# Kernel tuning notes

Measured on AMD Instinct MI355X. Metric: run time of the kernel, lower is better.

## Reference

```python
import jax, jax.numpy as jnp
import numpy as np

N_NODES = 100000


def gcn_conv(x, edge_index, W, b, n_nodes):
    """PyG GCNConv: add self-loops, symmetric deg^-1/2 normalization,
    linear transform, scatter-add aggregate, bias."""
    src, dst = edge_index[0], edge_index[1]
    # add self-loops
    loop = jnp.arange(n_nodes, dtype=edge_index.dtype)
    src = jnp.concatenate([src, loop])
    dst = jnp.concatenate([dst, loop])
    # transform first (in_dim >= out_dim ordering used by PyG)
    h = x @ W  # [N, out]
    # symmetric normalization from in-degree (incl. self-loops)
    ones = jnp.ones(src.shape[0], dtype=x.dtype)
    deg = jax.ops.segment_sum(ones, dst, num_segments=n_nodes)
    dinv = jnp.where(deg > 0, jax.lax.rsqrt(deg), 0.0).astype(x.dtype)
    norm = dinv[src] * dinv[dst]  # [E+N]
    msg = h[src] * norm[:, None]  # gather + scale
    out = jax.ops.segment_sum(msg, dst, num_segments=n_nodes)
    return out + b


def setup_inputs() -> dict:
    key = jax.random.key(0)
    k1, k2, k3, k4 = jax.random.split(key, 4)
    n, e = N_NODES, 1600000
    d_in, d_hid, n_cls = 256, 256, 64
    x = jax.random.normal(k1, (n, d_in), dtype=jnp.float32)
    edge_index = jax.random.randint(k2, (2, e), 0, n, dtype=jnp.int64)
    W1 = jax.random.normal(k3, (d_in, d_hid), dtype=jnp.float32) / np.sqrt(d_in)
    b1 = jnp.zeros((d_hid,), dtype=jnp.float32)
    W2 = jax.random.normal(k4, (d_hid, n_cls), dtype=jnp.float32) / np.sqrt(d_hid)
    b2 = jnp.zeros((n_cls,), dtype=jnp.float32)
    return {"x": x, "edge_index": edge_index, "W1": W1, "b1": b1, "W2": W2, "b2": b2}


def reference(x, edge_index, W1, b1, W2, b2):
    n = x.shape[0]
    h = jax.nn.relu(gcn_conv(x, edge_index, W1, b1, n))
    # dropout is identity in eval mode (training=False)
    logits = gcn_conv(h, edge_index, W2, b2, n)
    return jax.nn.log_softmax(logits, axis=1)
```

## Files before the change

kernel.cpp:

```cpp
#include <hip/hip_runtime.h>
#include <math.h>


typedef __attribute__((ext_vector_type(8))) short bf16x8;
typedef __attribute__((ext_vector_type(4))) float f32x4;

__device__ inline unsigned short f2bf(float f) {
    union { float f; unsigned int u; } v; v.f = f;
    unsigned int r = v.u + 0x7fffu + ((v.u >> 16) & 1u);
    return (unsigned short)(r >> 16);
}
__device__ inline float bf2f_lo(unsigned int u) {
    union { unsigned int u; float f; } v; v.u = u << 16; return v.f;
}
__device__ inline float bf2f_hi(unsigned int u) {
    union { unsigned int u; float f; } v; v.u = u & 0xffff0000u; return v.f;
}

__device__ inline void acc8(float* acc, uint4 q, float w) {
    acc[0] += bf2f_lo(q.x) * w; acc[1] += bf2f_hi(q.x) * w;
    acc[2] += bf2f_lo(q.y) * w; acc[3] += bf2f_hi(q.y) * w;
    acc[4] += bf2f_lo(q.z) * w; acc[5] += bf2f_hi(q.z) * w;
    acc[6] += bf2f_lo(q.w) * w; acc[7] += bf2f_hi(q.w) * w;
}

__global__ __launch_bounds__(256) void deg_rank_kernel(
    const int* __restrict__ dst, int E, int* __restrict__ cnt,
    int* __restrict__ rank) {
    int e = blockIdx.x * blockDim.x + threadIdx.x;
    if (e < E) rank[e] = atomicAdd(&cnt[dst[e]], 1);
}

__global__ __launch_bounds__(256) void scan_part1_kernel(
    const int* __restrict__ cnt, int* __restrict__ bsum, int N) {
    __shared__ int s[256];
    const int tid = threadIdx.x;
    int base = blockIdx.x * 1024 + tid * 4;
    int v = 0;
#pragma unroll
    for (int j = 0; j < 4; ++j)
        if (base + j < N) v += cnt[base + j];
    s[tid] = v;
    __syncthreads();
    for (int off = 128; off > 0; off >>= 1) {
        if (tid < off) s[tid] += s[tid + off];
        __syncthreads();
    }
    if (tid == 0) bsum[blockIdx.x] = s[0];
}

__global__ __launch_bounds__(1024) void scan_part2_kernel(
    const int* __restrict__ bsum, int* __restrict__ boffs, int NB,
    int* __restrict__ row_ptr, int N) {
    __shared__ int s[1024];
    const int tid = threadIdx.x;
    int v = (tid < NB) ? bsum[tid] : 0;
    s[tid] = v;
    __syncthreads();
    for (int off = 1; off < 1024; off <<= 1) {
        int t = (tid >= off) ? s[tid - off] : 0;
        __syncthreads();
        if (tid >= off) s[tid] += t;
        __syncthreads();
    }
    if (tid < NB) boffs[tid] = s[tid] - v;
    if (tid == 1023) row_ptr[N] = s[1023];
}

__global__ __launch_bounds__(256) void scan_part3_kernel(
    const int* __restrict__ cnt, const int* __restrict__ boffs,
    int* __restrict__ row_ptr, int N) {
    __shared__ int s[256];
    const int tid = threadIdx.x;
    int base = blockIdx.x * 1024 + tid * 4;
    int c[4];
    int v = 0;
#pragma unroll
    for (int j = 0; j < 4; ++j) {
        c[j] = (base + j < N) ? cnt[base + j] : 0;
        v += c[j];
    }
    s[tid] = v;
    __syncthreads();
    for (int off = 1; off < 256; off <<= 1) {
        int t = (tid >= off) ? s[tid - off] : 0;
        __syncthreads();
        if (tid >= off) s[tid] += t;
        __syncthreads();
    }
    int run = boffs[blockIdx.x] + s[tid] - v;
#pragma unroll
    for (int j = 0; j < 4; ++j) {
        if (base + j < N) {
            row_ptr[base + j] = run;
            run += c[j];
        }
    }
}

__global__ __launch_bounds__(256) void scatter_kernel(
    const int* __restrict__ src, const int* __restrict__ dst,
    const int* __restrict__ rank, const int* __restrict__ cnt,
    const int* __restrict__ row_ptr, int2* __restrict__ csr_ew, int E) {
    int e = blockIdx.x * blockDim.x + threadIdx.x;
    if (e >= E) return;
    int s = src[e], d = dst[e];
    float w = rsqrtf((float)cnt[s] + 1.0f) * rsqrtf((float)cnt[d] + 1.0f);
    int pos = row_ptr[d] + rank[e];
    int2 rec;
    rec.x = s;
    rec.y = __float_as_int(w);
    csr_ew[pos] = rec;
}

__global__ __launch_bounds__(256) void castw_kernel(
    const float* __restrict__ W1, const float* __restrict__ W2,
    unsigned short* __restrict__ W1t, unsigned short* __restrict__ W2t) {
    int i = blockIdx.x * 256 + threadIdx.x;
    if (i < 65536) {
        int n = i >> 8, k = i & 255;
        W1t[i] = f2bf(W1[(size_t)k * 256 + n]);
    } else if (i < 65536 + 16384) {
        int j = i - 65536;
        int n = j >> 8, k = j & 255;
        W2t[j] = f2bf(W2[(size_t)k * 64 + n]);
    }
}

__global__ __launch_bounds__(256) void gemm1_kernel(
    const float* __restrict__ A, const unsigned short* __restrict__ Bt,
    unsigned short* __restrict__ C, int M) {
    __shared__ unsigned short As[128][32];
    __shared__ unsigned short Bs[256][32];

    const int tid = threadIdx.x;
    const int wave = tid >> 6, lane = tid & 63;
    const int quad = lane >> 4, l15 = lane & 15;
    const int m0 = blockIdx.x * 128;

    f32x4 acc[8][4] = {};

    const int arow = tid >> 1;
    const int akk  = (tid & 1) << 4;
    const int gr = m0 + arow;

    for (int k0 = 0; k0 < 256; k0 += 32) {
        float4 a0 = make_float4(0.f,0.f,0.f,0.f), a1 = a0, a2 = a0, a3 = a0;
        if (gr < M) {
            const float* ap = &A[(size_t)gr * 256 + k0 + akk];
            a0 = *(const float4*)&ap[0];
            a1 = *(const float4*)&ap[4];
            a2 = *(const float4*)&ap[8];
            a3 = *(const float4*)&ap[12];
        }
        bf16x8 av0, av1;
        av0[0] = (short)f2bf(a0.x); av0[1] = (short)f2bf(a0.y);
        av0[2] = (short)f2bf(a0.z); av0[3] = (short)f2bf(a0.w);
        av0[4] = (short)f2bf(a1.x); av0[5] = (short)f2bf(a1.y);
        av0[6] = (short)f2bf(a1.z); av0[7] = (short)f2bf(a1.w);
        av1[0] = (short)f2bf(a2.x); av1[1] = (short)f2bf(a2.y);
        av1[2] = (short)f2bf(a2.z); av1[3] = (short)f2bf(a2.w);
        av1[4] = (short)f2bf(a3.x); av1[5] = (short)f2bf(a3.y);
        av1[6] = (short)f2bf(a3.z); av1[7] = (short)f2bf(a3.w);
        *(bf16x8*)&As[arow][akk]     = av0;
        *(bf16x8*)&As[arow][akk + 8] = av1;

        const unsigned short* bsrc = &Bt[(size_t)tid * 256 + k0];
        *(bf16x8*)&Bs[tid][0]  = *(const bf16x8*)&bsrc[0];
        *(bf16x8*)&Bs[tid][8]  = *(const bf16x8*)&bsrc[8];
        *(bf16x8*)&Bs[tid][16] = *(const bf16x8*)&bsrc[16];
        *(bf16x8*)&Bs[tid][24] = *(const bf16x8*)&bsrc[24];
        __syncthreads();

        bf16x8 bfv[4];
#pragma unroll
        for (int nt = 0; nt < 4; ++nt)
            bfv[nt] = *(const bf16x8*)&Bs[wave * 64 + nt * 16 + l15][quad * 8];
#pragma unroll
        for (int mt = 0; mt < 8; ++mt) {
            bf16x8 af = *(const bf16x8*)&As[mt * 16 + l15][quad * 8];
#pragma unroll
            for (int nt = 0; nt < 4; ++nt)
                acc[mt][nt] = __builtin_amdgcn_mfma_f32_16x16x32_bf16(
                    af, bfv[nt], acc[mt][nt], 0, 0, 0);
        }
        __syncthreads();
    }

#pragma unroll
    for (int mt = 0; mt < 8; ++mt) {
#pragma unroll
        for (int nt = 0; nt < 4; ++nt) {
            int gcol = wave * 64 + nt * 16 + l15;
#pragma unroll
            for (int r = 0; r < 4; ++r) {
                int grow = m0 + mt * 16 + quad * 4 + r;
                if (grow < M)
                    C[(size_t)grow * 256 + gcol] = f2bf(acc[mt][nt][r]);
            }
        }
    }
}

__global__ __launch_bounds__(256) void aggfused_kernel(
    const uint4* __restrict__ h,
    const int2* __restrict__ ew,
    const int* __restrict__ row_ptr, const int* __restrict__ cnt,
    const float* __restrict__ bias, const unsigned short* __restrict__ W2t,
    unsigned short* __restrict__ h2b, int N) {
    __shared__ unsigned short As[16][264];

    const int tid = threadIdx.x;
    const int wave = tid >> 6, lane = tid & 63;
    const int half = lane >> 5;
    const int c = lane & 31;
    const int node0 = blockIdx.x * 16;

    for (int i = 0; i < 4; ++i) {
        const int local = wave * 4 + i;
        const int node = node0 + local;
        float acc[8] = {0.f, 0.f, 0.f, 0.f, 0.f, 0.f, 0.f, 0.f};
        if (node < N) {
            float dv = rsqrtf((float)cnt[node] + 1.0f);
            float w0 = dv * dv;
            {
                uint4 q = h[(size_t)node * 32 + c];
                acc8(acc, q, half == 0 ? w0 : 0.f);
            }
            const int beg = row_ptr[node], end = row_ptr[node + 1];
            int e = beg;
            for (; e + 8 <= end; e += 8) {
                int2 r0 = ew[e + 0 + half];
                int2 r1 = ew[e + 2 + half];
                int2 r2 = ew[e + 4 + half];
                int2 r3 = ew[e + 6 + half];
                uint4 q0 = h[(size_t)r0.x * 32 + c];
                uint4 q1 = h[(size_t)r1.x * 32 + c];
                uint4 q2 = h[(size_t)r2.x * 32 + c];
                uint4 q3 = h[(size_t)r3.x * 32 + c];
                acc8(acc, q0, __int_as_float(r0.y));
                acc8(acc, q1, __int_as_float(r1.y));
                acc8(acc, q2, __int_as_float(r2.y));
                acc8(acc, q3, __int_as_float(r3.y));
            }
            for (; e < end; e += 2) {
                int idx = e + half;
                int idxc = min(idx, end - 1);
                int2 r = ew[idxc];
                float w = (idx < end) ? __int_as_float(r.y) : 0.f;
                uint4 q = h[(size_t)r.x * 32 + c];
                acc8(acc, q, w);
            }
        }
#pragma unroll
        for (int k = 0; k < 8; ++k) acc[k] += __shfl_xor(acc[k], 32, 64);

        if (half == 0) {
            float4 b0 = *(const float4*)&bias[c * 8];
            float4 b1 = *(const float4*)&bias[c * 8 + 4];
            unsigned int o0 = f2bf(fmaxf(acc[0] + b0.x, 0.f));
            unsigned int o1 = f2bf(fmaxf(acc[1] + b0.y, 0.f));
            unsigned int o2 = f2bf(fmaxf(acc[2] + b0.z, 0.f));
            unsigned int o3 = f2bf(fmaxf(acc[3] + b0.w, 0.f));
            unsigned int o4 = f2bf(fmaxf(acc[4] + b1.x, 0.f));
            unsigned int o5 = f2bf(fmaxf(acc[5] + b1.y, 0.f));
            unsigned int o6 = f2bf(fmaxf(acc[6] + b1.z, 0.f));
            unsigned int o7 = f2bf(fmaxf(acc[7] + b1.w, 0.f));
            uint4 ov;
            ov.x = o0 | (o1 << 16);
            ov.y = o2 | (o3 << 16);
            ov.z = o4 | (o5 << 16);
            ov.w = o6 | (o7 << 16);
            *(uint4*)&As[local][c * 8] = ov;
        }
    }
    __syncthreads();

    const int quad = lane >> 4, l15 = lane & 15;
    f32x4 accd = {};
#pragma unroll
    for (int k0 = 0; k0 < 8; ++k0) {
        bf16x8 af = *(const bf16x8*)&As[l15][k0 * 32 + quad * 8];
        bf16x8 bf = *(const bf16x8*)&W2t[(size_t)(wave * 16 + l15) * 256 +
                                         k0 * 32 + quad * 8];
        accd = __builtin_amdgcn_mfma_f32_16x16x32_bf16(af, bf, accd, 0, 0, 0);
    }
#pragma unroll
    for (int r = 0; r < 4; ++r) {
        int node = node0 + quad * 4 + r;
        if (node < N)
            h2b[(size_t)node * 64 + wave * 16 + l15] = f2bf(accd[r]);
    }
}

__global__ __launch_bounds__(256) void agg64_kernel(
    const uint4* __restrict__ h,
    const int2* __restrict__ ew, const int* __restrict__ row_ptr,
    const int* __restrict__ cnt, const float* __restrict__ bias,
    float* __restrict__ out, int N) {
    const int node = blockIdx.x * 4 + (threadIdx.x >> 6);
    if (node >= N) return;
    const int lane = threadIdx.x & 63;
    const int g = lane >> 3;
    const int c = lane & 7;

    float dv = rsqrtf((float)cnt[node] + 1.0f);
    float w0 = dv * dv;

    float acc[8] = {0.f, 0.f, 0.f, 0.f, 0.f, 0.f, 0.f, 0.f};
    {
        uint4 q = h[(size_t)node * 8 + c];
        acc8(acc, q, g == 0 ? w0 : 0.f);
    }

    const int beg = row_ptr[node], end = row_ptr[node + 1];
    int e = beg;
    for (; e + 16 <= end; e += 16) {
        int2 r0 = ew[e + g];
        int2 r1 = ew[e + 8 + g];
        uint4 q0 = h[(size_t)r0.x * 8 + c];
        uint4 q1 = h[(size_t)r1.x * 8 + c];
        acc8(acc, q0, __int_as_float(r0.y));
        acc8(acc, q1, __int_as_float(r1.y));
    }
    for (; e < end; e += 8) {
        int idx = e + g;
        int idxc = min(idx, end - 1);
        int2 r = ew[idxc];
        float w = (idx < end) ? __int_as_float(r.y) : 0.f;
        uint4 q = h[(size_t)r.x * 8 + c];
        acc8(acc, q, w);
    }

#pragma unroll
    for (int k = 0; k < 8; ++k) {
        acc[k] += __shfl_xor(acc[k], 8, 64);
        acc[k] += __shfl_xor(acc[k], 16, 64);
        acc[k] += __shfl_xor(acc[k], 32, 64);
    }

    float4 b0 = *(const float4*)&bias[c * 8];
    float4 b1 = *(const float4*)&bias[c * 8 + 4];
    float v[8];
    v[0] = acc[0] + b0.x; v[1] = acc[1] + b0.y;
    v[2] = acc[2] + b0.z; v[3] = acc[3] + b0.w;
    v[4] = acc[4] + b1.x; v[5] = acc[5] + b1.y;
    v[6] = acc[6] + b1.z; v[7] = acc[7] + b1.w;

    float m = v[0];
#pragma unroll
    for (int k = 1; k < 8; ++k) m = fmaxf(m, v[k]);
    m = fmaxf(m, __shfl_xor(m, 1, 64));
    m = fmaxf(m, __shfl_xor(m, 2, 64));
    m = fmaxf(m, __shfl_xor(m, 4, 64));
    float s = 0.f;
#pragma unroll
    for (int k = 0; k < 8; ++k) s += expf(v[k] - m);
    s += __shfl_xor(s, 1, 64);
    s += __shfl_xor(s, 2, 64);
    s += __shfl_xor(s, 4, 64);
    float ls = m + logf(s);

    if (g == 0) {
        float4 o0, o1;
        o0.x = v[0] - ls; o0.y = v[1] - ls; o0.z = v[2] - ls; o0.w = v[3] - ls;
        o1.x = v[4] - ls; o1.y = v[5] - ls; o1.z = v[6] - ls; o1.w = v[7] - ls;
        *(float4*)&out[(size_t)node * 64 + c * 8] = o0;
        *(float4*)&out[(size_t)node * 64 + c * 8 + 4] = o1;
    }
}

extern "C" void kernel_launch(void* const* d_in, const int* in_sizes, int n_in,
                              void* d_out, int out_size, void* d_ws, size_t ws_size,
                              hipStream_t stream) {
    const float* x  = (const float*)d_in[0];
    const int*   ei = (const int*)d_in[1];
    const float* W1 = (const float*)d_in[2];
    const float* b1 = (const float*)d_in[3];
    const float* W2 = (const float*)d_in[4];
    const float* b2 = (const float*)d_in[5];
    float* out = (float*)d_out;

    const int N = in_sizes[0] / 256;
    const int E = in_sizes[1] / 2;
    const int NP = 102400;
    const int NB = (N + 1023) / 1024;

    char* ws = (char*)d_ws;
    int*   cnt     = (int*)ws;                 ws += (size_t)NP * 4;
    int*   rank    = (int*)ws;                 ws += (size_t)E * 4;
    int*   row_ptr = (int*)ws;                 ws += (size_t)(NP + 4) * 4;
    int*   bsum    = (int*)ws;                 ws += (size_t)1024 * 4;
    int*   boffs   = (int*)ws;                 ws += (size_t)1024 * 4;
    int2*  csr_ew  = (int2*)ws;                ws += (size_t)E * 8;
    unsigned short* W1t   = (unsigned short*)ws; ws += (size_t)256 * 256 * 2;
    unsigned short* W2t   = (unsigned short*)ws; ws += (size_t)256 * 64 * 2;
    unsigned short* h1b   = (unsigned short*)ws; ws += (size_t)N * 256 * 2;
    unsigned short* h2b   = (unsigned short*)ws; ws += (size_t)N * 64 * 2;

    hipMemsetAsync(cnt, 0, (size_t)N * sizeof(int), stream);

    deg_rank_kernel<<<(E + 255) / 256, 256, 0, stream>>>(ei + E, E, cnt, rank);
    scan_part1_kernel<<<NB, 256, 0, stream>>>(cnt, bsum, N);
    scan_part2_kernel<<<1, 1024, 0, stream>>>(bsum, boffs, NB, row_ptr, N);
    scan_part3_kernel<<<NB, 256, 0, stream>>>(cnt, boffs, row_ptr, N);
    scatter_kernel<<<(E + 255) / 256, 256, 0, stream>>>(
        ei, ei + E, rank, cnt, row_ptr, csr_ew, E);

    castw_kernel<<<(65536 + 16384 + 255) / 256, 256, 0, stream>>>(W1, W2, W1t, W2t);

    gemm1_kernel<<<(N + 127) / 128, 256, 0, stream>>>(x, W1t, h1b, N);

    aggfused_kernel<<<(N + 15) / 16, 256, 0, stream>>>(
        (const uint4*)h1b, csr_ew, row_ptr, cnt, b1, W2t, h2b, N);

    agg64_kernel<<<(N + 3) / 4, 256, 0, stream>>>(
        (const uint4*)h2b, csr_ew, row_ptr, cnt, b2, out, N);
}
```

Measured before the change: 543.5 us.

## Aggregate bf16 x before W1 and fuse layer-1 GEMM into aggregation kernel

Reorders layer 1 to aggregate the bf16-cast input features first and then multiply by W1, which is valid because aggregation is linear. The separate GEMM kernel is removed: the x cast joins the weight-cast kernel, and the aggregation kernel now runs the W1 MFMA, bias+ReLU, and the W2 MFMA on each 16-node tile in shared memory. This drops the h1 write and read round-trip and one launch. In exchange each block re-reads W1t (128KB) from global/L2 per 16 nodes, and the bf16 rounding order changes.

```diff
diff --git a/kernel.cpp b/kernel.cpp
--- a/kernel.cpp
+++ b/kernel.cpp
@@ -113,102 +113,41 @@
     csr_ew[pos] = rec;
 }
 
-__global__ __launch_bounds__(256) void castw_kernel(
-    const float* __restrict__ W1, const float* __restrict__ W2,
-    unsigned short* __restrict__ W1t, unsigned short* __restrict__ W2t) {
+__global__ __launch_bounds__(256) void castxw_kernel(
+    const float* __restrict__ x, const float* __restrict__ W1,
+    const float* __restrict__ W2, unsigned int* __restrict__ xb,
+    unsigned short* __restrict__ W1t, unsigned short* __restrict__ W2t,
+    int NX8) {
     int i = blockIdx.x * 256 + threadIdx.x;
-    if (i < 65536) {
-        int n = i >> 8, k = i & 255;
-        W1t[i] = f2bf(W1[(size_t)k * 256 + n]);
-    } else if (i < 65536 + 16384) {
-        int j = i - 65536;
+    if (i < NX8) {
+        const float4* xp = (const float4*)&x[(size_t)i * 8];
+        float4 a0 = xp[0], a1 = xp[1];
+        uint4 o;
+        o.x = (unsigned int)f2bf(a0.x) | ((unsigned int)f2bf(a0.y) << 16);
+        o.y = (unsigned int)f2bf(a0.z) | ((unsigned int)f2bf(a0.w) << 16);
+        o.z = (unsigned int)f2bf(a1.x) | ((unsigned int)f2bf(a1.y) << 16);
+        o.w = (unsigned int)f2bf(a1.z) | ((unsigned int)f2bf(a1.w) << 16);
+        *(uint4*)&xb[(size_t)i * 4] = o;
+    } else if (i < NX8 + 65536) {
+        int j = i - NX8;
+        int n = j >> 8, k = j & 255;
+        W1t[j] = f2bf(W1[(size_t)k * 256 + n]);
+    } else if (i < NX8 + 65536 + 16384) {
+        int j = i - NX8 - 65536;
         int n = j >> 8, k = j & 255;
         W2t[j] = f2bf(W2[(size_t)k * 64 + n]);
     }
 }
 
-__global__ __launch_bounds__(256) void gemm1_kernel(
-    const float* __restrict__ A, const unsigned short* __restrict__ Bt,
-    unsigned short* __restrict__ C, int M) {
-    __shared__ unsigned short As[128][32];
-    __shared__ unsigned short Bs[256][32];
-
-    const int tid = threadIdx.x;
-    const int wave = tid >> 6, lane = tid & 63;
-    const int quad = lane >> 4, l15 = lane & 15;
-    const int m0 = blockIdx.x * 128;
-
-    f32x4 acc[8][4] = {};
-
-    const int arow = tid >> 1;
-    const int akk  = (tid & 1) << 4;
-    const int gr = m0 + arow;
-
-    for (int k0 = 0; k0 < 256; k0 += 32) {
-        float4 a0 = make_float4(0.f,0.f,0.f,0.f), a1 = a0, a2 = a0, a3 = a0;
-        if (gr < M) {
-            const float* ap = &A[(size_t)gr * 256 + k0 + akk];
-            a0 = *(const float4*)&ap[0];
-            a1 = *(const float4*)&ap[4];
-            a2 = *(const float4*)&ap[8];
-            a3 = *(const float4*)&ap[12];
-        }
-        bf16x8 av0, av1;
-        av0[0] = (short)f2bf(a0.x); av0[1] = (short)f2bf(a0.y);
-        av0[2] = (short)f2bf(a0.z); av0[3] = (short)f2bf(a0.w);
-        av0[4] = (short)f2bf(a1.x); av0[5] = (short)f2bf(a1.y);
-        av0[6] = (short)f2bf(a1.z); av0[7] = (short)f2bf(a1.w);
-        av1[0] = (short)f2bf(a2.x); av1[1] = (short)f2bf(a2.y);
-        av1[2] = (short)f2bf(a2.z); av1[3] = (short)f2bf(a2.w);
-        av1[4] = (short)f2bf(a3.x); av1[5] = (short)f2bf(a3.y);
-        av1[6] = (short)f2bf(a3.z); av1[7] = (short)f2bf(a3.w);
-        *(bf16x8*)&As[arow][akk]     = av0;
-        *(bf16x8*)&As[arow][akk + 8] = av1;
-
-        const unsigned short* bsrc = &Bt[(size_t)tid * 256 + k0];
-        *(bf16x8*)&Bs[tid][0]  = *(const bf16x8*)&bsrc[0];
-        *(bf16x8*)&Bs[tid][8]  = *(const bf16x8*)&bsrc[8];
-        *(bf16x8*)&Bs[tid][16] = *(const bf16x8*)&bsrc[16];
-        *(bf16x8*)&Bs[tid][24] = *(const bf16x8*)&bsrc[24];
-        __syncthreads();
-
-        bf16x8 bfv[4];
-#pragma unroll
-        for (int nt = 0; nt < 4; ++nt)
-            bfv[nt] = *(const bf16x8*)&Bs[wave * 64 + nt * 16 + l15][quad * 8];
-#pragma unroll
-        for (int mt = 0; mt < 8; ++mt) {
-            bf16x8 af = *(const bf16x8*)&As[mt * 16 + l15][quad * 8];
-#pragma unroll
-            for (int nt = 0; nt < 4; ++nt)
-                acc[mt][nt] = __builtin_amdgcn_mfma_f32_16x16x32_bf16(
-                    af, bfv[nt], acc[mt][nt], 0, 0, 0);
-        }
-        __syncthreads();
-    }
-
-#pragma unroll
-    for (int mt = 0; mt < 8; ++mt) {
-#pragma unroll
-        for (int nt = 0; nt < 4; ++nt) {
-            int gcol = wave * 64 + nt * 16 + l15;
-#pragma unroll
-            for (int r = 0; r < 4; ++r) {
-                int grow = m0 + mt * 16 + quad * 4 + r;
-                if (grow < M)
-                    C[(size_t)grow * 256 + gcol] = f2bf(acc[mt][nt][r]);
-            }
-        }
-    }
-}
-
-__global__ __launch_bounds__(256) void aggfused_kernel(
+__global__ __launch_bounds__(256) void megafused_kernel(
     const uint4* __restrict__ h,
     const int2* __restrict__ ew,
     const int* __restrict__ row_ptr, const int* __restrict__ cnt,
-    const float* __restrict__ bias, const unsigned short* __restrict__ W2t,
+    const float* __restrict__ b1, const unsigned short* __restrict__ W1t,
+    const unsigned short* __restrict__ W2t,
     unsigned short* __restrict__ h2b, int N) {
-    __shared__ unsigned short As[16][264];
+    __shared__ unsigned short r0[16][264];
+    __shared__ unsigned short r1[16][264];
 
     const int tid = threadIdx.x;
     const int wave = tid >> 6, lane = tid & 63;
@@ -230,18 +169,18 @@
             const int beg = row_ptr[node], end = row_ptr[node + 1];
             int e = beg;
             for (; e + 8 <= end; e += 8) {
-                int2 r0 = ew[e + 0 + half];
-                int2 r1 = ew[e + 2 + half];
-                int2 r2 = ew[e + 4 + half];
-                int2 r3 = ew[e + 6 + half];
-                uint4 q0 = h[(size_t)r0.x * 32 + c];
-                uint4 q1 = h[(size_t)r1.x * 32 + c];
-                uint4 q2 = h[(size_t)r2.x * 32 + c];
-                uint4 q3 = h[(size_t)r3.x * 32 + c];
-                acc8(acc, q0, __int_as_float(r0.y));
-                acc8(acc, q1, __int_as_float(r1.y));
-                acc8(acc, q2, __int_as_float(r2.y));
-                acc8(acc, q3, __int_as_float(r3.y));
+                int2 p0 = ew[e + 0 + half];
+                int2 p1 = ew[e + 2 + half];
+                int2 p2 = ew[e + 4 + half];
+                int2 p3 = ew[e + 6 + half];
+                uint4 q0 = h[(size_t)p0.x * 32 + c];
+                uint4 q1 = h[(size_t)p1.x * 32 + c];
+                uint4 q2 = h[(size_t)p2.x * 32 + c];
+                uint4 q3 = h[(size_t)p3.x * 32 + c];
+                acc8(acc, q0, __int_as_float(p0.y));
+                acc8(acc, q1, __int_as_float(p1.y));
+                acc8(acc, q2, __int_as_float(p2.y));
+                acc8(acc, q3, __int_as_float(p3.y));
             }
             for (; e < end; e += 2) {
                 int idx = e + half;
@@ -256,31 +195,47 @@
         for (int k = 0; k < 8; ++k) acc[k] += __shfl_xor(acc[k], 32, 64);
 
         if (half == 0) {
-            float4 b0 = *(const float4*)&bias[c * 8];
-            float4 b1 = *(const float4*)&bias[c * 8 + 4];
-            unsigned int o0 = f2bf(fmaxf(acc[0] + b0.x, 0.f));
-            unsigned int o1 = f2bf(fmaxf(acc[1] + b0.y, 0.f));
-            unsigned int o2 = f2bf(fmaxf(acc[2] + b0.z, 0.f));
-            unsigned int o3 = f2bf(fmaxf(acc[3] + b0.w, 0.f));
-            unsigned int o4 = f2bf(fmaxf(acc[4] + b1.x, 0.f));
-            unsigned int o5 = f2bf(fmaxf(acc[5] + b1.y, 0.f));
-            unsigned int o6 = f2bf(fmaxf(acc[6] + b1.z, 0.f));
-            unsigned int o7 = f2bf(fmaxf(acc[7] + b1.w, 0.f));
             uint4 ov;
-            ov.x = o0 | (o1 << 16);
-            ov.y = o2 | (o3 << 16);
-            ov.z = o4 | (o5 << 16);
-            ov.w = o6 | (o7 << 16);
-            *(uint4*)&As[local][c * 8] = ov;
+            ov.x = (unsigned int)f2bf(acc[0]) | ((unsigned int)f2bf(acc[1]) << 16);
+            ov.y = (unsigned int)f2bf(acc[2]) | ((unsigned int)f2bf(acc[3]) << 16);
+            ov.z = (unsigned int)f2bf(acc[4]) | ((unsigned int)f2bf(acc[5]) << 16);
+            ov.w = (unsigned int)f2bf(acc[6]) | ((unsigned int)f2bf(acc[7]) << 16);
+            *(uint4*)&r0[local][c * 8] = ov;
         }
     }
     __syncthreads();
 
     const int quad = lane >> 4, l15 = lane & 15;
+    {
+        f32x4 accb[4] = {};
+#pragma unroll
+        for (int k0 = 0; k0 < 8; ++k0) {
+            bf16x8 af = *(const bf16x8*)&r0[l15][k0 * 32 + quad * 8];
+#pragma unroll
+            for (int nt = 0; nt < 4; ++nt) {
+                bf16x8 bf = *(const bf16x8*)&W1t[
+                    (size_t)(wave * 64 + nt * 16 + l15) * 256 + k0 * 32 + quad * 8];
+                accb[nt] = __builtin_amdgcn_mfma_f32_16x16x32_bf16(
+                    af, bf, accb[nt], 0, 0, 0);
+            }
+        }
+#pragma unroll
+        for (int nt = 0; nt < 4; ++nt) {
+            int col = wave * 64 + nt * 16 + l15;
+            float bb = b1[col];
+#pragma unroll
+            for (int r = 0; r < 4; ++r) {
+                int row = quad * 4 + r;
+                r1[row][col] = f2bf(fmaxf(accb[nt][r] + bb, 0.f));
+            }
+        }
+    }
+    __syncthreads();
+
     f32x4 accd = {};
 #pragma unroll
     for (int k0 = 0; k0 < 8; ++k0) {
-        bf16x8 af = *(const bf16x8*)&As[l15][k0 * 32 + quad * 8];
+        bf16x8 af = *(const bf16x8*)&r1[l15][k0 * 32 + quad * 8];
         bf16x8 bf = *(const bf16x8*)&W2t[(size_t)(wave * 16 + l15) * 256 +
                                          k0 * 32 + quad * 8];
         accd = __builtin_amdgcn_mfma_f32_16x16x32_bf16(af, bf, accd, 0, 0, 0);
@@ -385,6 +340,7 @@
     const int E = in_sizes[1] / 2;
     const int NP = 102400;
     const int NB = (N + 1023) / 1024;
+    const int NX8 = N * 32;
 
     char* ws = (char*)d_ws;
     int*   cnt     = (int*)ws;                 ws += (size_t)NP * 4;
@@ -393,10 +349,10 @@
     int*   bsum    = (int*)ws;                 ws += (size_t)1024 * 4;
     int*   boffs   = (int*)ws;                 ws += (size_t)1024 * 4;
     int2*  csr_ew  = (int2*)ws;                ws += (size_t)E * 8;
-    unsigned short* W1t   = (unsigned short*)ws; ws += (size_t)256 * 256 * 2;
-    unsigned short* W2t   = (unsigned short*)ws; ws += (size_t)256 * 64 * 2;
-    unsigned short* h1b   = (unsigned short*)ws; ws += (size_t)N * 256 * 2;
-    unsigned short* h2b   = (unsigned short*)ws; ws += (size_t)N * 64 * 2;
+    unsigned short* W1t = (unsigned short*)ws; ws += (size_t)256 * 256 * 2;
+    unsigned short* W2t = (unsigned short*)ws; ws += (size_t)256 * 64 * 2;
+    unsigned short* xb  = (unsigned short*)ws; ws += (size_t)N * 256 * 2;
+    unsigned short* h2b = (unsigned short*)ws; ws += (size_t)N * 64 * 2;
 
     hipMemsetAsync(cnt, 0, (size_t)N * sizeof(int), stream);
 
@@ -407,12 +363,11 @@
     scatter_kernel<<<(E + 255) / 256, 256, 0, stream>>>(
         ei, ei + E, rank, cnt, row_ptr, csr_ew, E);
 
-    castw_kernel<<<(65536 + 16384 + 255) / 256, 256, 0, stream>>>(W1, W2, W1t, W2t);
-
-    gemm1_kernel<<<(N + 127) / 128, 256, 0, stream>>>(x, W1t, h1b, N);
-
-    aggfused_kernel<<<(N + 15) / 16, 256, 0, stream>>>(
-        (const uint4*)h1b, csr_ew, row_ptr, cnt, b1, W2t, h2b, N);
+    castxw_kernel<<<(NX8 + 65536 + 16384 + 255) / 256, 256, 0, stream>>>(
+        x, W1, W2, (unsigned int*)xb, W1t, W2t, NX8);
+
+    megafused_kernel<<<(N + 15) / 16, 256, 0, stream>>>(
+        (const uint4*)xb, csr_ew, row_ptr, cnt, b1, W1t, W2t, h2b, N);
 
     agg64_kernel<<<(N + 3) / 4, 256, 0, stream>>>(
         (const uint4*)h2b, csr_ew, row_ptr, cnt, b2, out, N);
```

Result: slower. 583.7 us (+7.4%).
